# Kernel optimization log

Hardware: AMD Instinct MI355X
Metric: run time of the kernel (lower is better)

## Reference

```python
import jax, jax.numpy as jnp
import numpy as np

B, T, E, H = 2, 2048, 1024, 16
D = E // H  # head dim = 64
ROPE_BASE = 10000.0


def setup_inputs() -> dict:
    key = jax.random.key(0)
    k0, k1, k2 = jax.random.split(key, 3)
    s = 0.02  # GPT-style init scale
    return {
        "x": jax.random.normal(k0, (B, T, E), jnp.float32),
        "w_qkv": jax.random.normal(k1, (E, 3 * E), jnp.float32) * s,
        "b_qkv": jnp.zeros((3 * E,), jnp.float32),
        "w_out": jax.random.normal(k2, (E, E), jnp.float32) * s,
        "b_out": jnp.zeros((E,), jnp.float32),
    }


def _rope_tables(t, d, dtype):
    # Llama rotary with scale=1 (YaRN degenerates to vanilla RoPE)
    inv_freq = 1.0 / (ROPE_BASE ** (jnp.arange(0, d, 2, dtype=jnp.float32) / d))
    freqs = jnp.arange(t, dtype=jnp.float32)[:, None] * inv_freq[None, :]  # [T, D/2]
    emb = jnp.concatenate([freqs, freqs], axis=-1)  # [T, D]
    return jnp.cos(emb).astype(dtype), jnp.sin(emb).astype(dtype)


def _rotate_half(x):
    return jnp.concatenate([-x[..., D // 2:], x[..., : D // 2]], axis=-1)


def reference(x, w_qkv, b_qkv, w_out, b_out):
    # 1) fused QKV projection
    qkv = x @ w_qkv + b_qkv                      # [B, T, 3E]
    q, k, v = jnp.split(qkv, 3, axis=-1)

    def heads(t):
        return t.reshape(B, T, H, D).transpose(0, 2, 1, 3)  # [B, H, T, D]

    q, k, v = heads(q), heads(k), heads(v)

    # 2) rotary position embedding on q, k
    cos, sin = _rope_tables(T, D, x.dtype)       # [T, D], broadcasts over B, H
    q = q * cos + _rotate_half(q) * sin
    k = k * cos + _rotate_half(k) * sin

    # 3) causal scaled dot-product attention
    scale = jnp.asarray(1.0 / np.sqrt(D), x.dtype)
    scores = jnp.einsum("bhqd,bhkd->bhqk", q, k) * scale
    causal = jnp.tril(jnp.ones((T, T), dtype=bool))
    scores = jnp.where(causal, scores, jnp.finfo(scores.dtype).min)
    attn = jax.nn.softmax(scores, axis=-1)
    out = jnp.einsum("bhqk,bhkd->bhqd", attn, v)  # [B, H, T, D]

    # 4) merge heads + output projection
    out = out.transpose(0, 2, 1, 3).reshape(B, T, E)
    return out @ w_out + b_out
```

## Files before the change

### kernel.cpp

```cpp
#include <hip/hip_runtime.h>
#include <hip/hip_bf16.h>
#include <stdint.h>

#define B_  2
#define T_  2048
#define E_  1024
#define H_  16
#define D_  64
#define BH_ 32

typedef unsigned short ushort_t;
typedef __attribute__((ext_vector_type(8))) short bfrag;
typedef __attribute__((ext_vector_type(4))) short s16x4;
typedef __attribute__((ext_vector_type(4))) float f32x4;

__device__ __forceinline__ ushort_t f2b(float f) {
    uint32_t u = __builtin_bit_cast(uint32_t, f);
    u += 0x7fffu + ((u >> 16) & 1u);
    return (ushort_t)(u >> 16);
}

#if defined(__has_builtin)
#if __has_builtin(__builtin_amdgcn_exp2f)
#define EXP2(x) __builtin_amdgcn_exp2f(x)
#endif
#endif
#ifndef EXP2
__device__ __forceinline__ float hexp2_(float x) {
    float r;
    asm volatile("v_exp_f32 %0, %1\n\ts_nop 1" : "=v"(r) : "v"(x));
    return r;
}
#define EXP2(x) hexp2_(x)
#endif

__device__ __forceinline__ uint32_t cvtpk_bf16(float lo, float hi) {
    uint32_t r;
    asm("v_cvt_pk_bf16_f32 %0, %1, %2" : "=v"(r) : "v"(lo), "v"(hi));
    return r;
}

typedef const __attribute__((address_space(1))) uint8_t* gas_t;
typedef __attribute__((address_space(3))) uint8_t* las_t;
__device__ __forceinline__ void gload_lds16(const void* g, void* l) {
    __builtin_amdgcn_global_load_lds((gas_t)g, (las_t)l, 16, 0, 0);
}
__device__ __forceinline__ void drain_vmem() {
    asm volatile("s_waitcnt vmcnt(0)" ::: "memory");
    __builtin_amdgcn_sched_barrier(0);
}

__global__ __launch_bounds__(256) void prep_kernel(const float* __restrict__ x, const float* __restrict__ w_qkv,
                                                   const float* __restrict__ w_out, ushort_t* __restrict__ xb,
                                                   ushort_t* __restrict__ wqkvT, ushort_t* __restrict__ woutT,
                                                   float2* __restrict__ cstab) {
    __shared__ float tile[32][36];
    int blk = blockIdx.x, tid = threadIdx.x;
    if (blk < 256) {
        int id = blk * 256 + tid;
        int j = id & 31, t = id >> 5;
        float ang = (float)t * expf(-(float)j * 0.2878231366242558f);
        float s, c;
        sincosf(ang, &s, &c);
        cstab[id] = make_float2(c, s);
    } else if (blk < 2304) {
        int i = ((blk - 256) * 256 + tid) * 8;
        float4 a = *(const float4*)(x + i);
        float4 b = *(const float4*)(x + i + 4);
        ushort_t r[8] = {f2b(a.x), f2b(a.y), f2b(a.z), f2b(a.w), f2b(b.x), f2b(b.y), f2b(b.z), f2b(b.w)};
        *(uint4*)(xb + i) = *(const uint4*)r;
    } else {
        const float* in;
        ushort_t* out;
        int R, C, bx, by;
        if (blk < 5376) { in = w_qkv; out = wqkvT; R = 1024; C = 3072; int t = blk - 2304; bx = t % 96; by = t / 96; }
        else            { in = w_out; out = woutT; R = 1024; C = 1024; int t = blk - 5376; bx = t % 32; by = t / 32; }
        int c0 = bx * 32, r0 = by * 32;
        int ty = tid >> 3, tx = tid & 7;
        float4 v = *(const float4*)&in[(size_t)(r0 + ty) * C + c0 + tx * 4];
        *(float4*)&tile[ty][tx * 4] = v;
        __syncthreads();
        int cc = tid & 31, rq = tid >> 5;
        float t0 = tile[rq * 4 + 0][cc], t1 = tile[rq * 4 + 1][cc];
        float t2 = tile[rq * 4 + 2][cc], t3 = tile[rq * 4 + 3][cc];
        uint2 w;
        w.x = cvtpk_bf16(t0, t1);
        w.y = cvtpk_bf16(t2, t3);
        *(uint2*)&out[(size_t)(c0 + cc) * R + r0 + rq * 4] = w;
    }
}

__global__ __launch_bounds__(256) void gemm_qkv_kernel(const ushort_t* __restrict__ A, const ushort_t* __restrict__ Bt,
                                                       const float* __restrict__ bias, const float2* __restrict__ cstab,
                                                       ushort_t* __restrict__ qw, ushort_t* __restrict__ kw,
                                                       ushort_t* __restrict__ vw) {
    const int K = 1024;
    __shared__ ushort_t As[128 * 128];
    __shared__ ushort_t Bs[128 * 128];
    int tid = threadIdx.x, lane = tid & 63, wid = tid >> 6;
    int lm = lane & 15, lg = lane >> 4;
    int bid = blockIdx.x;
    int xcd = bid & 7, idx = bid >> 3;
    int bm = xcd * 4 + idx / 24;
    int bn = idx % 24;
    int wm = wid >> 1, wn = wid & 1;

    int cbase = bn * 128 + wn * 64;
    bool qk = (cbase < 2048);

    f32x4 acc[4][4] = {};
    const ushort_t* ag = A + (size_t)bm * 128 * K;
    const ushort_t* bg = Bt + (size_t)bn * 128 * K;

    for (int kt = 0; kt < K / 128; ++kt) {
        __syncthreads();
#pragma unroll
        for (int c = 0; c < 8; ++c) {
            int G = c * 256 + tid;
            int rr = G >> 4;
            int slot = G & 15;
            int gs = (slot & 8) | ((slot & 7) ^ (rr & 7));
            gload_lds16(ag + (size_t)rr * K + kt * 128 + gs * 8, As + (c * 256 + wid * 64) * 8);
            gload_lds16(bg + (size_t)rr * K + kt * 128 + gs * 8, Bs + (c * 256 + wid * 64) * 8);
        }
        __syncthreads();
#pragma unroll
        for (int kk = 0; kk < 4; ++kk) {
            bfrag a[4], b[4];
#pragma unroll
            for (int mi = 0; mi < 4; ++mi) {
                int row = wm * 64 + mi * 16 + lm;
                int slot = kk * 4 + lg;
                int phys = (slot & 8) | ((slot & 7) ^ (lm & 7));
                a[mi] = *(const bfrag*)&As[row * 128 + phys * 8];
            }
#pragma unroll
            for (int ni = 0; ni < 4; ++ni) {
                int row = wn * 64 + ni * 16 + lm;
                int slot = kk * 4 + lg;
                int phys = (slot & 8) | ((slot & 7) ^ (lm & 7));
                b[ni] = *(const bfrag*)&Bs[row * 128 + phys * 8];
            }
            if (qk) {
#pragma unroll
                for (int mi = 0; mi < 4; ++mi)
#pragma unroll
                    for (int ni = 0; ni < 4; ++ni)
                        acc[mi][ni] = __builtin_amdgcn_mfma_f32_16x16x32_bf16(b[ni], a[mi], acc[mi][ni], 0, 0, 0);
            } else {
#pragma unroll
                for (int mi = 0; mi < 4; ++mi)
#pragma unroll
                    for (int ni = 0; ni < 4; ++ni)
                        acc[mi][ni] = __builtin_amdgcn_mfma_f32_16x16x32_bf16(a[mi], b[ni], acc[mi][ni], 0, 0, 0);
            }
        }
    }

    int sel = cbase >> 10;
    int h = (cbase & 1023) >> 6;
    if (qk) {
        ushort_t* dst = sel ? kw : qw;
        float scale = sel ? 1.0f : 0.18033688011112042f;
        float4 bias4[4];
#pragma unroll
        for (int ni = 0; ni < 4; ++ni)
            bias4[ni] = *(const float4*)&bias[cbase + ni * 16 + lg * 4];
#pragma unroll
        for (int mi = 0; mi < 4; ++mi) {
            int r = bm * 128 + wm * 64 + mi * 16 + lm;
            int bb = r >> 11, t = r & (T_ - 1);
            size_t rowbase = ((size_t)(bb * H_ + h) * T_ + t) * D_;
#pragma unroll
            for (int nip = 0; nip < 2; ++nip) {
                const float4* cs2 = (const float4*)(cstab + t * 32 + nip * 16 + lg * 4);
                float4 ca = cs2[0], cb = cs2[1];
                float xl[4], xh[4];
#pragma unroll
                for (int i = 0; i < 4; ++i) {
                    xl[i] = acc[mi][nip][i]     + ((const float*)&bias4[nip])[i];
                    xh[i] = acc[mi][nip + 2][i] + ((const float*)&bias4[nip + 2])[i];
                }
                float rl0 = (xl[0] * ca.x - xh[0] * ca.y) * scale;
                float rl1 = (xl[1] * ca.z - xh[1] * ca.w) * scale;
                float rl2 = (xl[2] * cb.x - xh[2] * cb.y) * scale;
                float rl3 = (xl[3] * cb.z - xh[3] * cb.w) * scale;
                float rh0 = (xh[0] * ca.x + xl[0] * ca.y) * scale;
                float rh1 = (xh[1] * ca.z + xl[1] * ca.w) * scale;
                float rh2 = (xh[2] * cb.x + xl[2] * cb.y) * scale;
                float rh3 = (xh[3] * cb.z + xl[3] * cb.w) * scale;
                uint2 wlo, whi;
                wlo.x = cvtpk_bf16(rl0, rl1); wlo.y = cvtpk_bf16(rl2, rl3);
                whi.x = cvtpk_bf16(rh0, rh1); whi.y = cvtpk_bf16(rh2, rh3);
                *(uint2*)&dst[rowbase + nip * 16 + lg * 4]      = wlo;
                *(uint2*)&dst[rowbase + 32 + nip * 16 + lg * 4] = whi;
            }
        }
    } else {
        float bb4[4];
#pragma unroll
        for (int ni = 0; ni < 4; ++ni) bb4[ni] = bias[cbase + ni * 16 + lm];
#pragma unroll
        for (int ni = 0; ni < 4; ++ni) {
            int d = ni * 16 + lm;
#pragma unroll
            for (int mi = 0; mi < 4; ++mi) {
                int r = bm * 128 + wm * 64 + mi * 16 + lg * 4;
                int bb = r >> 11, tq = r & (T_ - 1);
                uint2 w;
                w.x = cvtpk_bf16(acc[mi][ni][0] + bb4[ni], acc[mi][ni][1] + bb4[ni]);
                w.y = cvtpk_bf16(acc[mi][ni][2] + bb4[ni], acc[mi][ni][3] + bb4[ni]);
                *(uint2*)&vw[((size_t)(bb * H_ + h) * D_ + d) * T_ + tq] = w;
            }
        }
    }
}

__global__ __launch_bounds__(256, 2) void flash_kernel(const ushort_t* __restrict__ q, const ushort_t* __restrict__ k,
                                                       const ushort_t* __restrict__ vt, ushort_t* __restrict__ o) {
    __shared__ ushort_t smemK[256 * 64];
    __shared__ ushort_t smemV[64 * 256];
    int tid = threadIdx.x, lane = tid & 63, wid = tid >> 6;
    int lm = lane & 15, lg = lane >> 4;
    int x = blockIdx.x & 7, r = blockIdx.x >> 3;
    int half = r >> 5, idx = r & 31;
    int bh = x * 4 + (idx & 3);
    int jq = idx >> 2;
    int j = half ? jq : 15 - jq;
    int q0w = j * 128 + wid * 32;
    int b = bh >> 4, h = bh & 15;
    int nt = (j >> 1) + 1;

    const ushort_t* qb = q + (size_t)bh * T_ * D_;
    const ushort_t* kb = k + (size_t)bh * T_ * D_;
    const ushort_t* vb = vt + (size_t)bh * D_ * T_;

    bfrag aq[2][2];
#pragma unroll
    for (int s = 0; s < 2; ++s)
#pragma unroll
        for (int hh = 0; hh < 2; ++hh)
            aq[s][hh] = *(const bfrag*)(qb + (size_t)(q0w + s * 16 + lm) * D_ + hh * 32 + lg * 8);

    f32x4 acc[2][4] = {};
    float lsum[2] = {0.f, 0.f};

    for (int t = 0; t < nt; ++t) {
        int k0 = t * 256;
        __syncthreads();
#pragma unroll
        for (int c = 0; c < 8; ++c) {
            int G = c * 256 + tid;
            int rrk = G >> 3, gk = (G & 7) ^ (rrk & 7);
            gload_lds16(kb + (size_t)(k0 + rrk) * D_ + gk * 8, smemK + (c * 256 + wid * 64) * 8);
            int rrv = G >> 5, gv = (G & 31) ^ (rrv & 7);
            gload_lds16(vb + (size_t)rrv * T_ + k0 + gv * 8, smemV + (c * 256 + wid * 64) * 8);
        }
        drain_vmem();
        __syncthreads();

        for (int h1 = 0; h1 < 4; ++h1) {
            int hk0 = k0 + h1 * 64;
            if (hk0 > q0w + 31) continue;
            bfrag ka[4][2];
#pragma unroll
            for (int sb = 0; sb < 4; ++sb)
#pragma unroll
                for (int hh = 0; hh < 2; ++hh) {
                    int krr = h1 * 64 + sb * 16 + lm;
                    int gr = (hh * 4 + lg) ^ (krr & 7);
                    ka[sb][hh] = *(const bfrag*)&smemK[krr * 64 + gr * 8];
                }
            s16x4 vq[4][4];
#pragma unroll
            for (int qq = 0; qq < 4; ++qq)
#pragma unroll
                for (int db = 0; db < 4; ++db) {
                    int rr = db * 16 + lm;
                    int g = h1 * 8 + qq * 2 + (lg >> 1);
                    int p = g ^ (rr & 7);
                    vq[qq][db] = *(const s16x4*)&smemV[rr * 256 + p * 8 + (lg & 1) * 4];
                }
            f32x4 st[2][4];
#pragma unroll
            for (int s = 0; s < 2; ++s)
#pragma unroll
                for (int sb = 0; sb < 4; ++sb) {
                    f32x4 z = {};
                    z = __builtin_amdgcn_mfma_f32_16x16x32_bf16(ka[sb][0], aq[s][0], z, 0, 0, 0);
                    st[s][sb] = __builtin_amdgcn_mfma_f32_16x16x32_bf16(ka[sb][1], aq[s][1], z, 0, 0, 0);
                }
            if (hk0 + 63 > q0w) {
#pragma unroll
                for (int s = 0; s < 2; ++s)
#pragma unroll
                    for (int sb = 0; sb < 4; ++sb)
#pragma unroll
                        for (int i = 0; i < 4; ++i)
                            if (hk0 + sb * 16 + lg * 4 + i > q0w + s * 16 + lm) st[s][sb][i] = -1e30f;
            }
#pragma unroll
            for (int s = 0; s < 2; ++s) {
                float pv[4][4];
#pragma unroll
                for (int sb = 0; sb < 4; ++sb)
#pragma unroll
                    for (int i = 0; i < 4; ++i)
                        pv[sb][i] = EXP2(st[s][sb][i]);
                lsum[s] += ((pv[0][0] + pv[0][1]) + (pv[0][2] + pv[0][3])) +
                           ((pv[1][0] + pv[1][1]) + (pv[1][2] + pv[1][3])) +
                           ((pv[2][0] + pv[2][1]) + (pv[2][2] + pv[2][3])) +
                           ((pv[3][0] + pv[3][1]) + (pv[3][2] + pv[3][3]));
                uint4 u0, u1;
                u0.x = cvtpk_bf16(pv[0][0], pv[0][1]);
                u0.y = cvtpk_bf16(pv[0][2], pv[0][3]);
                u0.z = cvtpk_bf16(pv[1][0], pv[1][1]);
                u0.w = cvtpk_bf16(pv[1][2], pv[1][3]);
                u1.x = cvtpk_bf16(pv[2][0], pv[2][1]);
                u1.y = cvtpk_bf16(pv[2][2], pv[2][3]);
                u1.z = cvtpk_bf16(pv[3][0], pv[3][1]);
                u1.w = cvtpk_bf16(pv[3][2], pv[3][3]);
                bfrag pf0 = __builtin_bit_cast(bfrag, u0);
                bfrag pf1 = __builtin_bit_cast(bfrag, u1);
#pragma unroll
                for (int db = 0; db < 4; ++db) {
                    bfrag va01 = __builtin_shufflevector(vq[0][db], vq[1][db], 0, 1, 2, 3, 4, 5, 6, 7);
                    bfrag va23 = __builtin_shufflevector(vq[2][db], vq[3][db], 0, 1, 2, 3, 4, 5, 6, 7);
                    acc[s][db] = __builtin_amdgcn_mfma_f32_16x16x32_bf16(va01, pf0, acc[s][db], 0, 0, 0);
                    acc[s][db] = __builtin_amdgcn_mfma_f32_16x16x32_bf16(va23, pf1, acc[s][db], 0, 0, 0);
                }
            }
        }
    }

#pragma unroll
    for (int s = 0; s < 2; ++s) {
        float lM = lsum[s];
        lM += __shfl_xor(lM, 16);
        lM += __shfl_xor(lM, 32);
        float inv = 1.0f / lM;
        int tq = q0w + s * 16 + lm;
        size_t ro = ((size_t)b * T_ + tq) * E_ + h * D_;
#pragma unroll
        for (int db = 0; db < 4; ++db) {
            uint2 w;
            w.x = cvtpk_bf16(acc[s][db][0] * inv, acc[s][db][1] * inv);
            w.y = cvtpk_bf16(acc[s][db][2] * inv, acc[s][db][3] * inv);
            *(uint2*)(o + ro + db * 16 + lg * 4) = w;
        }
    }
}

__global__ __launch_bounds__(256) void gemm_out_kernel(const ushort_t* __restrict__ A, const ushort_t* __restrict__ Bt,
                                                       const float* __restrict__ bias, float* __restrict__ out) {
    const int K = 1024;
    __shared__ ushort_t As[2][128 * 64];
    __shared__ ushort_t Bs[2][64 * 64];
    int tid = threadIdx.x, lane = tid & 63, wid = tid >> 6;
    int lm = lane & 15, lg = lane >> 4;
    int bid = blockIdx.x;
    int xcd = bid & 7, idx = bid >> 3;
    int bm = xcd * 4 + idx / 16;
    int bn = idx % 16;

    f32x4 acc[2][4] = {};
    const ushort_t* ag = A + (size_t)bm * 128 * K;
    const ushort_t* bg = Bt + (size_t)bn * 64 * K;

#define OUT_STAGE(kt_, buf_)                                                              \
    _Pragma("unroll")                                                                     \
    for (int c = 0; c < 4; ++c) {                                                         \
        int G = c * 256 + tid;                                                            \
        int rr = G >> 3;                                                                  \
        int gs = (G & 7) ^ (rr & 7);                                                      \
        gload_lds16(ag + (size_t)rr * K + (kt_) * 64 + gs * 8, &As[buf_][(c * 256 + wid * 64) * 8]); \
    }                                                                                     \
    _Pragma("unroll")                                                                     \
    for (int c = 0; c < 2; ++c) {                                                         \
        int G = c * 256 + tid;                                                            \
        int rr = G >> 3;                                                                  \
        int gs = (G & 7) ^ (rr & 7);                                                      \
        gload_lds16(bg + (size_t)rr * K + (kt_) * 64 + gs * 8, &Bs[buf_][(c * 256 + wid * 64) * 8]); \
    }

    int cur = 0;
    OUT_STAGE(0, 0);
    drain_vmem();
    __syncthreads();

    for (int kt = 0; kt < K / 64; ++kt) {
        if (kt + 1 < K / 64) { OUT_STAGE(kt + 1, cur ^ 1); }
        bfrag a[2][2], b[2][4];
#pragma unroll
        for (int kk = 0; kk < 2; ++kk) {
#pragma unroll
            for (int mi = 0; mi < 2; ++mi) {
                int row = wid * 32 + mi * 16 + lm;
                int slot = (kk * 4 + lg) ^ (lm & 7);
                a[kk][mi] = *(const bfrag*)&As[cur][row * 64 + slot * 8];
            }
#pragma unroll
            for (int ni = 0; ni < 4; ++ni) {
                int row = ni * 16 + lm;
                int slot = (kk * 4 + lg) ^ (lm & 7);
                b[kk][ni] = *(const bfrag*)&Bs[cur][row * 64 + slot * 8];
            }
        }
#pragma unroll
        for (int kk = 0; kk < 2; ++kk)
#pragma unroll
            for (int mi = 0; mi < 2; ++mi)
#pragma unroll
                for (int ni = 0; ni < 4; ++ni)
                    acc[mi][ni] = __builtin_amdgcn_mfma_f32_16x16x32_bf16(a[kk][mi], b[kk][ni], acc[mi][ni], 0, 0, 0);
        drain_vmem();
        __syncthreads();
        cur ^= 1;
    }
#undef OUT_STAGE

#pragma unroll
    for (int ni = 0; ni < 4; ++ni) {
        int c = bn * 64 + ni * 16 + lm;
        float bb = bias[c];
#pragma unroll
        for (int mi = 0; mi < 2; ++mi) {
#pragma unroll
            for (int i = 0; i < 4; ++i) {
                int r = bm * 128 + wid * 32 + mi * 16 + lg * 4 + i;
                out[(size_t)r * 1024 + c] = acc[mi][ni][i] + bb;
            }
        }
    }
}

extern "C" void kernel_launch(void* const* d_in, const int* in_sizes, int n_in,
                              void* d_out, int out_size, void* d_ws, size_t ws_size,
                              hipStream_t stream) {
    const float* x     = (const float*)d_in[0];
    const float* w_qkv = (const float*)d_in[1];
    const float* b_qkv = (const float*)d_in[2];
    const float* w_out = (const float*)d_in[3];
    const float* b_out = (const float*)d_in[4];
    float* out = (float*)d_out;

    ushort_t* ws    = (ushort_t*)d_ws;
    ushort_t* xb    = ws;
    ushort_t* wqkvT = xb + 4194304;
    ushort_t* woutT = wqkvT + 3145728;
    ushort_t* qw    = woutT + 1048576;
    ushort_t* kw    = qw + 4194304;
    ushort_t* vw    = kw + 4194304;
    ushort_t* ao    = vw + 4194304;
    float2*   cstab = (float2*)(ao + 4194304);

    prep_kernel<<<dim3(6400), 256, 0, stream>>>(x, w_qkv, w_out, xb, wqkvT, woutT, cstab);
    gemm_qkv_kernel<<<dim3(768), 256, 0, stream>>>(xb, wqkvT, b_qkv, cstab, qw, kw, vw);
    flash_kernel<<<dim3(512), 256, 0, stream>>>(qw, kw, vw, ao);
    gemm_out_kernel<<<dim3(512), 256, 0, stream>>>(ao, woutT, b_out, out);
}
```

Baseline: 102.1 us.

## Replace double-buffered K=64 staging with single-buffer K=128 tiles in output GEMM

The output-projection GEMM drops its double-buffered 64-wide K pipeline and instead loads a single 128-wide K tile per iteration, with a swizzle adapted to the wider rows. This halves the number of loop iterations and barrier pairs and keeps the LDS footprint the same. It loses the overlap of the next tile's global loads with the current MFMA work, so every iteration now waits on its own loads. Note that no explicit vmem drain appears before the second barrier, which may leave the loaded data unsynchronised unless __syncthreads covers the async LDS loads.

```diff
diff --git a/kernel.cpp b/kernel.cpp
--- a/kernel.cpp
+++ b/kernel.cpp
@@ -354,8 +354,8 @@
 __global__ __launch_bounds__(256) void gemm_out_kernel(const ushort_t* __restrict__ A, const ushort_t* __restrict__ Bt,
                                                        const float* __restrict__ bias, float* __restrict__ out) {
     const int K = 1024;
-    __shared__ ushort_t As[2][128 * 64];
-    __shared__ ushort_t Bs[2][64 * 64];
+    __shared__ ushort_t As[128 * 128];
+    __shared__ ushort_t Bs[64 * 128];
     int tid = threadIdx.x, lane = tid & 63, wid = tid >> 6;
     int lm = lane & 15, lg = lane >> 4;
     int bid = blockIdx.x;
@@ -367,57 +367,49 @@
     const ushort_t* ag = A + (size_t)bm * 128 * K;
     const ushort_t* bg = Bt + (size_t)bn * 64 * K;
 
-#define OUT_STAGE(kt_, buf_)                                                              \
-    _Pragma("unroll")                                                                     \
-    for (int c = 0; c < 4; ++c) {                                                         \
-        int G = c * 256 + tid;                                                            \
-        int rr = G >> 3;                                                                  \
-        int gs = (G & 7) ^ (rr & 7);                                                      \
-        gload_lds16(ag + (size_t)rr * K + (kt_) * 64 + gs * 8, &As[buf_][(c * 256 + wid * 64) * 8]); \
-    }                                                                                     \
-    _Pragma("unroll")                                                                     \
-    for (int c = 0; c < 2; ++c) {                                                         \
-        int G = c * 256 + tid;                                                            \
-        int rr = G >> 3;                                                                  \
-        int gs = (G & 7) ^ (rr & 7);                                                      \
-        gload_lds16(bg + (size_t)rr * K + (kt_) * 64 + gs * 8, &Bs[buf_][(c * 256 + wid * 64) * 8]); \
-    }
-
-    int cur = 0;
-    OUT_STAGE(0, 0);
-    drain_vmem();
-    __syncthreads();
-
-    for (int kt = 0; kt < K / 64; ++kt) {
-        if (kt + 1 < K / 64) { OUT_STAGE(kt + 1, cur ^ 1); }
-        bfrag a[2][2], b[2][4];
-#pragma unroll
-        for (int kk = 0; kk < 2; ++kk) {
+    for (int kt = 0; kt < K / 128; ++kt) {
+        __syncthreads();
+#pragma unroll
+        for (int c = 0; c < 8; ++c) {
+            int G = c * 256 + tid;
+            int rr = G >> 4;
+            int slot = G & 15;
+            int gs = (slot & 8) | ((slot & 7) ^ (rr & 7));
+            gload_lds16(ag + (size_t)rr * K + kt * 128 + gs * 8, As + (c * 256 + wid * 64) * 8);
+        }
+#pragma unroll
+        for (int c = 0; c < 4; ++c) {
+            int G = c * 256 + tid;
+            int rr = G >> 4;
+            int slot = G & 15;
+            int gs = (slot & 8) | ((slot & 7) ^ (rr & 7));
+            gload_lds16(bg + (size_t)rr * K + kt * 128 + gs * 8, Bs + (c * 256 + wid * 64) * 8);
+        }
+        __syncthreads();
+#pragma unroll
+        for (int kk = 0; kk < 4; ++kk) {
+            bfrag a[2], b[4];
 #pragma unroll
             for (int mi = 0; mi < 2; ++mi) {
                 int row = wid * 32 + mi * 16 + lm;
-                int slot = (kk * 4 + lg) ^ (lm & 7);
-                a[kk][mi] = *(const bfrag*)&As[cur][row * 64 + slot * 8];
+                int slot = kk * 4 + lg;
+                int phys = (slot & 8) | ((slot & 7) ^ (lm & 7));
+                a[mi] = *(const bfrag*)&As[row * 128 + phys * 8];
             }
 #pragma unroll
             for (int ni = 0; ni < 4; ++ni) {
                 int row = ni * 16 + lm;
-                int slot = (kk * 4 + lg) ^ (lm & 7);
-                b[kk][ni] = *(const bfrag*)&Bs[cur][row * 64 + slot * 8];
-            }
-        }
-#pragma unroll
-        for (int kk = 0; kk < 2; ++kk)
+                int slot = kk * 4 + lg;
+                int phys = (slot & 8) | ((slot & 7) ^ (lm & 7));
+                b[ni] = *(const bfrag*)&Bs[row * 128 + phys * 8];
+            }
 #pragma unroll
             for (int mi = 0; mi < 2; ++mi)
 #pragma unroll
                 for (int ni = 0; ni < 4; ++ni)
-                    acc[mi][ni] = __builtin_amdgcn_mfma_f32_16x16x32_bf16(a[kk][mi], b[kk][ni], acc[mi][ni], 0, 0, 0);
-        drain_vmem();
-        __syncthreads();
-        cur ^= 1;
-    }
-#undef OUT_STAGE
+                    acc[mi][ni] = __builtin_amdgcn_mfma_f32_16x16x32_bf16(a[mi], b[ni], acc[mi][ni], 0, 0, 0);
+        }
+    }
 
 #pragma unroll
     for (int ni = 0; ni < 4; ++ni) {
```

Result: faster. 99.32 us, median of 2 (-2.7%).
